# Kernel tuning notes

Hardware: AMD Instinct MI355X
Metric: run time of the kernel (lower is better)

## Reference

```python
import jax, jax.numpy as jnp
import numpy as np

N_IN = 8192
C_IN, C_H, C_OUT = 64, 32, 32
L = 3
GRID = 64  # parent grid extent (parents live on even coords of a 128^3 grid)


def _build_coords_and_maps():
    """Build sparse voxel coords and the 27-offset kernel map for 3x3x3 stride-1 convs."""
    rng = np.random.RandomState(0)
    pts = rng.randint(0, GRID, size=(4 * N_IN, 3))
    uniq = np.unique(pts, axis=0)
    parents = uniq[rng.permutation(uniq.shape[0])[:N_IN]] * 2  # stride-2 coords in [0,128)
    offs = np.array([[i, j, k] for i in (0, 1) for j in (0, 1) for k in (0, 1)])
    # generative conv transpose kernel=2 stride=2: child k of parent i sits at row i*8+k
    coords = (parents[:, None, :] + offs[None]).reshape(-1, 3)
    n_out = coords.shape[0]
    D = 2 * GRID
    grid = -np.ones((D, D, D), dtype=np.int64)
    grid[coords[:, 0], coords[:, 1], coords[:, 2]] = np.arange(n_out)
    k_offs = np.array([[i, j, k] for i in (-1, 0, 1) for j in (-1, 0, 1) for k in (-1, 0, 1)])
    ins, outs = [], []
    for d in k_offs:
        sh = coords + d
        valid = np.all((sh >= 0) & (sh < D), axis=1)
        j = -np.ones(n_out, dtype=np.int64)
        j[valid] = grid[sh[valid, 0], sh[valid, 1], sh[valid, 2]]
        m = j >= 0
        ins.append(j[m])
        outs.append(np.nonzero(m)[0])
    P = max(len(a) for a in ins)
    nbr_in = np.full((27, P), n_out, dtype=np.int32)   # pad -> dummy zero row
    nbr_out = np.full((27, P), n_out, dtype=np.int32)  # pad -> dummy dropped row
    for k in range(27):
        nbr_in[k, : len(ins[k])] = ins[k]
        nbr_out[k, : len(outs[k])] = outs[k]
    return jnp.asarray(nbr_in), jnp.asarray(nbr_out), n_out


def setup_inputs() -> dict:
    nbr_in, nbr_out, n_out = _build_coords_and_maps()
    key = jax.random.key(0)
    ks = jax.random.split(key, 20)
    w = lambda k, shape, fan: jax.random.normal(k, shape, jnp.float32) / np.float32(np.sqrt(fan))
    C4, C2 = C_OUT // 4, C_OUT // 2
    inp = {
        "x": jax.random.normal(ks[0], (N_IN, C_IN), jnp.float32),
        "W_up": w(ks[1], (8, C_IN, C_H), C_IN),
        "b_up": 0.01 * jax.random.normal(ks[2], (C_H,), jnp.float32),
        "W_conv": w(ks[3], (27, C_H, C_OUT), 27 * C_H),
        "b_conv": 0.01 * jax.random.normal(ks[4], (C_OUT,), jnp.float32),
        "Wb00": w(ks[5], (L, 27, C_OUT, C4), 27 * C_OUT),
        "bb00": 0.01 * jax.random.normal(ks[6], (L, C4), jnp.float32),
        "Wb01": w(ks[7], (L, 27, C4, C2), 27 * C4),
        "bb01": 0.01 * jax.random.normal(ks[8], (L, C2), jnp.float32),
        "Wb10": w(ks[9], (L, C_OUT, C4), C_OUT),
        "bb10": 0.01 * jax.random.normal(ks[10], (L, C4), jnp.float32),
        "Wb11": w(ks[11], (L, 27, C4, C4), 27 * C4),
        "bb11": 0.01 * jax.random.normal(ks[12], (L, C4), jnp.float32),
        "Wb12": w(ks[13], (L, C4, C2), C4),
        "bb12": 0.01 * jax.random.normal(ks[14], (L, C2), jnp.float32),
        "W_cls": w(ks[15], (27, C_OUT, 1), 27 * C_OUT),
        "b_cls": 0.01 * jax.random.normal(ks[16], (1,), jnp.float32),
        "nbr_in": nbr_in,
        "nbr_out": nbr_out,
        # ground-truth occupancy of out coords in target_label (precomputed set membership)
        "target": jax.random.bernoulli(ks[17], 0.5, (n_out,)),
    }
    return inp


def reference(x, W_up, b_up, W_conv, b_conv, Wb00, bb00, Wb01, bb01,
              Wb10, bb10, Wb11, bb11, Wb12, bb12, W_cls, b_cls,
              nbr_in, nbr_out, target):
    n_out = target.shape[0]
    r = jax.nn.relu

    def sconv(f, W, b):
        # 3x3x3 stride-1 sparse conv via shared kernel map: gather -> per-offset GEMM -> scatter-add
        fpad = jnp.concatenate([f, jnp.zeros((1, f.shape[1]), f.dtype)], axis=0)
        g = fpad[nbr_in]                                   # [27, P, Cin]
        contrib = jnp.einsum('kpc,kcd->kpd', g, W)         # [27, P, Cout]
        out = jnp.zeros((n_out + 1, W.shape[2]), f.dtype)
        out = out.at[nbr_out.reshape(-1)].add(contrib.reshape(-1, W.shape[2]))
        return out[:n_out] + b

    # generative transpose kernel=2 stride=2: child k of parent i -> row i*8+k
    up = (jnp.einsum('nc,kcd->nkd', x, W_up) + b_up).reshape(n_out, -1)
    out = r(sconv(r(up), W_conv, b_conv))
    for l in range(L):  # InceptionResNet blocks (PCGCv2-style)
        p0 = sconv(r(sconv(out, Wb00[l], bb00[l])), Wb01[l], bb01[l])
        p1 = r(out @ Wb10[l] + bb10[l])
        p1 = r(sconv(p1, Wb11[l], bb11[l]))
        p1 = p1 @ Wb12[l] + bb12[l]
        out = jnp.concatenate([p0, p1], axis=-1) + out
    out_cls = sconv(out, W_cls, b_cls)                     # [n_out, 1]
    score = out_cls[:, 0]
    keep = score > 0
    # topk(.,1) fallback when everything is negative
    fallback = keep | (jnp.arange(n_out) == jnp.argmax(score))
    keep = jnp.where(jnp.max(score) < 0, fallback, keep)
    # MinkowskiPruning with static shapes: zero-mask pruned rows
    out_pruned = out * keep[:, None].astype(out.dtype)
    return out_pruned, out_cls, target, keep
```

## Files before the change

### kernel.cpp

```cpp
#include <hip/hip_runtime.h>
#include <math.h>

static inline int cdiv(long long a, int b){ return (int)((a + b - 1) / b); }
#define DEVINL __device__ __forceinline__

DEVINL float4 relu4(const float* a){
  return make_float4(fmaxf(a[0],0.f), fmaxf(a[1],0.f), fmaxf(a[2],0.f), fmaxf(a[3],0.f));
}

DEVINL void load32(float* fv, const float* __restrict__ p){
#pragma unroll
  for (int q = 0; q < 8; ++q){
    float4 v = ((const float4*)p)[q];
    fv[4*q]=v.x; fv[4*q+1]=v.y; fv[4*q+2]=v.z; fv[4*q+3]=v.w;
  }
}
DEVINL void load8(float* fv, const float* __restrict__ p){
#pragma unroll
  for (int q = 0; q < 2; ++q){
    float4 v = ((const float4*)p)[q];
    fv[4*q]=v.x; fv[4*q+1]=v.y; fv[4*q+2]=v.z; fv[4*q+3]=v.w;
  }
}

DEVINL int sib_k(int o, int op){
  return 13 + 9*(((op>>2)&1) - ((o>>2)&1))
            + 3*(((op>>1)&1) - ((o>>1)&1))
            +   ((op&1) - (o&1));
}

__global__ void k_rinit(int* __restrict__ cnt, int n){
  int i = blockIdx.x*blockDim.x + threadIdx.x;
  if (i < n) cnt[i] = 0;
}

__global__ void k_rbuild(const int* __restrict__ nin, const int* __restrict__ nout,
                         int* __restrict__ cnt, int* __restrict__ rem, int P, int N){
  int p = blockIdx.x*blockDim.x + threadIdx.x;
  if (p >= 27*P) return;
  int oi = nout[p];
  if (oi >= N) return;
  int j = nin[p];
  if ((oi >> 3) == (j >> 3)) return;
  int k = p / P;
  int pos = atomicAdd(&cnt[oi], 1);
  rem[(size_t)oi*20 + pos] = (j << 5) | k;
}

__global__ __launch_bounds__(256) void k_up(const float* __restrict__ x,
    const float* __restrict__ Wup, const float* __restrict__ bup,
    float* __restrict__ f, int Nn){
  __shared__ float Ws[64*32];
  const int kk = blockIdx.y;
  for (int e = threadIdx.x*4; e < 2048; e += 1024)
    *(float4*)&Ws[e] = *(const float4*)&Wup[(size_t)kk*2048 + e];
  __syncthreads();
  int t = threadIdx.x, cg = t & 7, nr = t >> 3;
  int n = blockIdx.x*32 + nr, c0 = cg*4;
  float4 b4 = *(const float4*)(bup + c0);
  float acc[4] = {b4.x, b4.y, b4.z, b4.w};
  float xr[64];
  const float4* xp = (const float4*)(x + (size_t)n*64);
#pragma unroll
  for (int q = 0; q < 16; ++q){
    float4 v = xp[q];
    xr[4*q]=v.x; xr[4*q+1]=v.y; xr[4*q+2]=v.z; xr[4*q+3]=v.w;
  }
#pragma unroll
  for (int cc = 0; cc < 64; ++cc){
    float4 w = *(const float4*)(Ws + cc*32 + c0);
    acc[0]=fmaf(xr[cc],w.x,acc[0]); acc[1]=fmaf(xr[cc],w.y,acc[1]);
    acc[2]=fmaf(xr[cc],w.z,acc[2]); acc[3]=fmaf(xr[cc],w.w,acc[3]);
  }
  *(float4*)(f + ((size_t)n*8 + kk)*32 + c0) = relu4(acc);
}

__global__ __launch_bounds__(512) void k_conv1(const float* __restrict__ fin,
    const float* __restrict__ Wg, const float* __restrict__ bg,
    const int* __restrict__ cnt, const int* __restrict__ rem,
    float* __restrict__ fout, int N){
  __shared__ float Ws[27*516];
  const int ch = blockIdx.y;
  int t = threadIdx.x;
  for (int m = t; m < 3456; m += 512){
    int k = m >> 7, r = m & 127, cc = r >> 2, q = r & 3;
    *(float4*)&Ws[k*516 + cc*16 + q*4] =
      *(const float4*)&Wg[((size_t)(k*32 + cc))*32 + ch*16 + q*4];
  }
  __syncthreads();
  int cg = t & 3, r = t >> 2;
  int row = blockIdx.x*128 + r;
  int o = row & 7, base = row & ~7, c0 = cg*4;
  float4 b4 = *(const float4*)(bg + ch*16 + c0);
  float acc[4] = {b4.x,b4.y,b4.z,b4.w};
  float fv[32];
#pragma unroll
  for (int op = 0; op < 8; ++op){
    int kk = sib_k(o, op);
    load32(fv, fin + (size_t)(base+op)*32);
    const float* wk = Ws + kk*516 + c0;
#pragma unroll
    for (int cc = 0; cc < 32; ++cc){
      float4 w = *(const float4*)(wk + cc*16);
      acc[0]=fmaf(fv[cc],w.x,acc[0]); acc[1]=fmaf(fv[cc],w.y,acc[1]);
      acc[2]=fmaf(fv[cc],w.z,acc[2]); acc[3]=fmaf(fv[cc],w.w,acc[3]);
    }
  }
  int nrm = cnt[row];
  for (int s = 0; s < nrm; ++s){
    int e = rem[(size_t)row*20 + s];
    int kk = e & 31, j = e >> 5;
    load32(fv, fin + (size_t)j*32);
    const float* wk = Ws + kk*516 + c0;
#pragma unroll
    for (int cc = 0; cc < 32; ++cc){
      float4 w = *(const float4*)(wk + cc*16);
      acc[0]=fmaf(fv[cc],w.x,acc[0]); acc[1]=fmaf(fv[cc],w.y,acc[1]);
      acc[2]=fmaf(fv[cc],w.z,acc[2]); acc[3]=fmaf(fv[cc],w.w,acc[3]);
    }
  }
  *(float4*)(fout + (size_t)row*32 + ch*16 + c0) = relu4(acc);
}

__global__ __launch_bounds__(256) void k_blk_a(const float* __restrict__ fO,
    const float* __restrict__ W00, const float* __restrict__ b00,
    const float* __restrict__ W10, const float* __restrict__ b10,
    const int* __restrict__ cnt, const int* __restrict__ rem,
    float* __restrict__ a8, float* __restrict__ b8, int N){
  __shared__ float Ws[27*260 + 256];
  int t = threadIdx.x;
  for (int m = t; m < 1728; m += 256){
    int k = m >> 6, r = m & 63, cc = r >> 1, q = r & 1;
    *(float4*)&Ws[k*260 + cc*8 + q*4] = ((const float4*)W00)[m];
  }
  if (t < 64) *(float4*)&Ws[27*260 + t*4] = ((const float4*)W10)[t];
  __syncthreads();
  int cg = t & 1, r = t >> 1;
  int row = blockIdx.x*128 + r;
  int o = row & 7, base = row & ~7, c0 = cg*4;
  float4 b4 = *(const float4*)(b00 + c0);
  float acc[4] = {b4.x,b4.y,b4.z,b4.w};
  float fv[32];
#pragma unroll
  for (int op = 0; op < 8; ++op){
    int kk = sib_k(o, op);
    load32(fv, fO + (size_t)(base+op)*32);
    const float* wk = Ws + kk*260 + c0;
#pragma unroll
    for (int cc = 0; cc < 32; ++cc){
      float4 w = *(const float4*)(wk + cc*8);
      acc[0]=fmaf(fv[cc],w.x,acc[0]); acc[1]=fmaf(fv[cc],w.y,acc[1]);
      acc[2]=fmaf(fv[cc],w.z,acc[2]); acc[3]=fmaf(fv[cc],w.w,acc[3]);
    }
  }
  int nrm = cnt[row];
  for (int s = 0; s < nrm; ++s){
    int e = rem[(size_t)row*20 + s];
    int kk = e & 31, j = e >> 5;
    load32(fv, fO + (size_t)j*32);
    const float* wk = Ws + kk*260 + c0;
#pragma unroll
    for (int cc = 0; cc < 32; ++cc){
      float4 w = *(const float4*)(wk + cc*8);
      acc[0]=fmaf(fv[cc],w.x,acc[0]); acc[1]=fmaf(fv[cc],w.y,acc[1]);
      acc[2]=fmaf(fv[cc],w.z,acc[2]); acc[3]=fmaf(fv[cc],w.w,acc[3]);
    }
  }
  *(float4*)(a8 + (size_t)row*8 + c0) = relu4(acc);
  load32(fv, fO + (size_t)row*32);
  float4 d4 = *(const float4*)(b10 + c0);
  float accb[4] = {d4.x,d4.y,d4.z,d4.w};
#pragma unroll
  for (int cc = 0; cc < 32; ++cc){
    float4 w = *(const float4*)(Ws + 27*260 + cc*8 + c0);
    accb[0]=fmaf(fv[cc],w.x,accb[0]); accb[1]=fmaf(fv[cc],w.y,accb[1]);
    accb[2]=fmaf(fv[cc],w.z,accb[2]); accb[3]=fmaf(fv[cc],w.w,accb[3]);
  }
  *(float4*)(b8 + (size_t)row*8 + c0) = relu4(accb);
}

__global__ __launch_bounds__(256) void k_blk_b(const float* __restrict__ a8,
    const float* __restrict__ b8,
    const float* __restrict__ W01, const float* __restrict__ b01,
    const float* __restrict__ W11, const float* __restrict__ b11,
    const float* __restrict__ W12, const float* __restrict__ b12,
    const int* __restrict__ cnt, const int* __restrict__ rem,
    float* __restrict__ fout, int N){
  __shared__ float Ws[27*132 + 27*68 + 128];
  int t = threadIdx.x;
  for (int m = t; m < 864; m += 256){
    int k = m >> 5, r = m & 31, cc = r >> 2, q = r & 3;
    *(float4*)&Ws[k*132 + cc*16 + q*4] = ((const float4*)W01)[m];
  }
  for (int m = t; m < 432; m += 256){
    int k = m >> 4, r = m & 15, cc = r >> 1, q = r & 1;
    *(float4*)&Ws[3564 + k*68 + cc*8 + q*4] = ((const float4*)W11)[m];
  }
  if (t < 32) *(float4*)&Ws[5400 + t*4] = ((const float4*)W12)[t];
  __syncthreads();
  int cg = t & 3, r = t >> 2;
  int row = blockIdx.x*64 + r;
  int o = row & 7, base = row & ~7, c0 = cg*4;
  float4 b4 = *(const float4*)(b01 + c0);
  float acc0[4] = {b4.x,b4.y,b4.z,b4.w};
  float t8[8];
#pragma unroll
  for (int c = 0; c < 8; ++c) t8[c] = b11[c];
  float av[8], bv[8];
#pragma unroll
  for (int op = 0; op < 8; ++op){
    int kk = sib_k(o, op);
    load8(av, a8 + (size_t)(base+op)*8);
    load8(bv, b8 + (size_t)(base+op)*8);
    const float* w01k = Ws + kk*132 + c0;
    const float* w11k = Ws + 3564 + kk*68;
#pragma unroll
    for (int cc = 0; cc < 8; ++cc){
      float4 w = *(const float4*)(w01k + cc*16);
      acc0[0]=fmaf(av[cc],w.x,acc0[0]); acc0[1]=fmaf(av[cc],w.y,acc0[1]);
      acc0[2]=fmaf(av[cc],w.z,acc0[2]); acc0[3]=fmaf(av[cc],w.w,acc0[3]);
      float4 u0 = *(const float4*)(w11k + cc*8);
      float4 u1 = *(const float4*)(w11k + cc*8 + 4);
      t8[0]=fmaf(bv[cc],u0.x,t8[0]); t8[1]=fmaf(bv[cc],u0.y,t8[1]);
      t8[2]=fmaf(bv[cc],u0.z,t8[2]); t8[3]=fmaf(bv[cc],u0.w,t8[3]);
      t8[4]=fmaf(bv[cc],u1.x,t8[4]); t8[5]=fmaf(bv[cc],u1.y,t8[5]);
      t8[6]=fmaf(bv[cc],u1.z,t8[6]); t8[7]=fmaf(bv[cc],u1.w,t8[7]);
    }
  }
  int nrm = cnt[row];
  for (int s = 0; s < nrm; ++s){
    int e = rem[(size_t)row*20 + s];
    int kk = e & 31, j = e >> 5;
    load8(av, a8 + (size_t)j*8);
    load8(bv, b8 + (size_t)j*8);
    const float* w01k = Ws + kk*132 + c0;
    const float* w11k = Ws + 3564 + kk*68;
#pragma unroll
    for (int cc = 0; cc < 8; ++cc){
      float4 w = *(const float4*)(w01k + cc*16);
      acc0[0]=fmaf(av[cc],w.x,acc0[0]); acc0[1]=fmaf(av[cc],w.y,acc0[1]);
      acc0[2]=fmaf(av[cc],w.z,acc0[2]); acc0[3]=fmaf(av[cc],w.w,acc0[3]);
      float4 u0 = *(const float4*)(w11k + cc*8);
      float4 u1 = *(const float4*)(w11k + cc*8 + 4);
      t8[0]=fmaf(bv[cc],u0.x,t8[0]); t8[1]=fmaf(bv[cc],u0.y,t8[1]);
      t8[2]=fmaf(bv[cc],u0.z,t8[2]); t8[3]=fmaf(bv[cc],u0.w,t8[3]);
      t8[4]=fmaf(bv[cc],u1.x,t8[4]); t8[5]=fmaf(bv[cc],u1.y,t8[5]);
      t8[6]=fmaf(bv[cc],u1.z,t8[6]); t8[7]=fmaf(bv[cc],u1.w,t8[7]);
    }
  }
#pragma unroll
  for (int c = 0; c < 8; ++c) t8[c] = fmaxf(t8[c], 0.f);
  float4 d4 = *(const float4*)(b12 + c0);
  float acc1[4] = {d4.x,d4.y,d4.z,d4.w};
#pragma unroll
  for (int cc = 0; cc < 8; ++cc){
    float4 w = *(const float4*)(Ws + 5400 + cc*16 + c0);
    acc1[0]=fmaf(t8[cc],w.x,acc1[0]); acc1[1]=fmaf(t8[cc],w.y,acc1[1]);
    acc1[2]=fmaf(t8[cc],w.z,acc1[2]); acc1[3]=fmaf(t8[cc],w.w,acc1[3]);
  }
  float4* o0 = (float4*)(fout + (size_t)row*32 + c0);
  float4* o1 = (float4*)(fout + (size_t)row*32 + 16 + c0);
  float4 v0 = *o0, v1 = *o1;
  v0.x+=acc0[0]; v0.y+=acc0[1]; v0.z+=acc0[2]; v0.w+=acc0[3];
  v1.x+=acc1[0]; v1.y+=acc1[1]; v1.z+=acc1[2]; v1.w+=acc1[3];
  *o0 = v0; *o1 = v1;
}

__global__ __launch_bounds__(256) void k_cls(const float* __restrict__ fO,
    const float* __restrict__ Wc, const float* __restrict__ bc,
    const int* __restrict__ cnt, const int* __restrict__ rem,
    float* __restrict__ cls, int N){
  __shared__ float Ws[27*36];
  int t = threadIdx.x;
  if (t < 216){
    int k = t >> 3, r = t & 7;
    *(float4*)&Ws[k*36 + r*4] = ((const float4*)Wc)[t];
  }
  __syncthreads();
  int row = blockIdx.x*256 + t;
  int o = row & 7, base = row & ~7;
  float acc = 0.f;
  float fv[32];
#pragma unroll
  for (int op = 0; op < 8; ++op){
    int kk = sib_k(o, op);
    load32(fv, fO + (size_t)(base+op)*32);
    const float* wk = Ws + kk*36;
#pragma unroll
    for (int c4 = 0; c4 < 8; ++c4){
      float4 w = *(const float4*)(wk + c4*4);
      acc = fmaf(fv[4*c4],w.x,acc);   acc = fmaf(fv[4*c4+1],w.y,acc);
      acc = fmaf(fv[4*c4+2],w.z,acc); acc = fmaf(fv[4*c4+3],w.w,acc);
    }
  }
  int nrm = cnt[row];
  for (int s = 0; s < nrm; ++s){
    int e = rem[(size_t)row*20 + s];
    int kk = e & 31, j = e >> 5;
    load32(fv, fO + (size_t)j*32);
    const float* wk = Ws + kk*36;
#pragma unroll
    for (int c4 = 0; c4 < 8; ++c4){
      float4 w = *(const float4*)(wk + c4*4);
      acc = fmaf(fv[4*c4],w.x,acc);   acc = fmaf(fv[4*c4+1],w.y,acc);
      acc = fmaf(fv[4*c4+2],w.z,acc); acc = fmaf(fv[4*c4+3],w.w,acc);
    }
  }
  cls[row] = acc + bc[0];
}

__global__ void k_reduce1(const float* __restrict__ s, float* __restrict__ pmax,
                          int* __restrict__ pidx, int n){
  __shared__ float sm[256]; __shared__ int si[256];
  int t = threadIdx.x;
  float v = -INFINITY; int vi = 0x7fffffff;
  for (int j = blockIdx.x*256 + t; j < n; j += gridDim.x*256){
    float w = s[j];
    if (w > v){ v = w; vi = j; }
  }
  sm[t] = v; si[t] = vi; __syncthreads();
  for (int o = 128; o > 0; o >>= 1){
    if (t < o){
      if (sm[t+o] > sm[t] || (sm[t+o] == sm[t] && si[t+o] < si[t])){ sm[t]=sm[t+o]; si[t]=si[t+o]; }
    }
    __syncthreads();
  }
  if (t == 0){ pmax[blockIdx.x] = sm[0]; pidx[blockIdx.x] = si[0]; }
}

__global__ void k_reduce2(const float* __restrict__ pmax, const int* __restrict__ pidx,
                          float* __restrict__ g, int nb){
  __shared__ float sm[256]; __shared__ int si[256];
  int t = threadIdx.x;
  sm[t] = (t < nb) ? pmax[t] : -INFINITY;
  si[t] = (t < nb) ? pidx[t] : 0x7fffffff;
  __syncthreads();
  for (int o = 128; o > 0; o >>= 1){
    if (t < o){
      if (sm[t+o] > sm[t] || (sm[t+o] == sm[t] && si[t+o] < si[t])){ sm[t]=sm[t+o]; si[t]=si[t+o]; }
    }
    __syncthreads();
  }
  if (t == 0){ g[0] = sm[0]; ((int*)g)[1] = si[0]; }
}

__global__ void k_final(const float* __restrict__ out, const float* __restrict__ cls,
                        const int* __restrict__ target, const float* __restrict__ g,
                        float* __restrict__ dout, int n_out){
  int idx = blockIdx.x*blockDim.x + threadIdx.x;
  if (idx >= n_out*32) return;
  int row = idx >> 5, c = idx & 31;
  float s = cls[row];
  bool keep = s > 0.f;
  if (g[0] < 0.f) keep = keep || (row == ((const int*)g)[1]);
  float km = keep ? 1.f : 0.f;
  dout[idx] = out[idx] * km;
  if (c == 0){
    dout[(size_t)n_out*32 + row] = s;
    dout[(size_t)n_out*33 + row] = (target[row] != 0) ? 1.f : 0.f;
    dout[(size_t)n_out*34 + row] = km;
  }
}

extern "C" void kernel_launch(void* const* d_in, const int* in_sizes, int n_in,
                              void* d_out, int out_size, void* d_ws, size_t ws_size,
                              hipStream_t stream){
  const float* x      = (const float*)d_in[0];
  const float* W_up   = (const float*)d_in[1];
  const float* b_up   = (const float*)d_in[2];
  const float* W_conv = (const float*)d_in[3];
  const float* b_conv = (const float*)d_in[4];
  const float* Wb00   = (const float*)d_in[5];
  const float* bb00   = (const float*)d_in[6];
  const float* Wb01   = (const float*)d_in[7];
  const float* bb01   = (const float*)d_in[8];
  const float* Wb10   = (const float*)d_in[9];
  const float* bb10   = (const float*)d_in[10];
  const float* Wb11   = (const float*)d_in[11];
  const float* bb11   = (const float*)d_in[12];
  const float* Wb12   = (const float*)d_in[13];
  const float* bb12   = (const float*)d_in[14];
  const float* W_cls  = (const float*)d_in[15];
  const float* b_cls  = (const float*)d_in[16];
  const int*   nbr_in = (const int*)d_in[17];
  const int*   nbr_out= (const int*)d_in[18];
  const int*   target = (const int*)d_in[19];

  const int N = in_sizes[19];
  const int P = in_sizes[17] / 27;
  const int pairsT = 27 * P;
  const int Nn = N / 8;

  int*   cnt  = (int*)d_ws;
  int*   rem  = cnt + N;
  float* wsf  = (float*)(rem + (size_t)N*20);
  float* f_tmp = wsf;
  float* f_out = f_tmp + (size_t)N*32;
  float* a8    = f_out + (size_t)N*32;
  float* b8    = a8 + (size_t)N*8;
  float* cls   = b8 + (size_t)N*8;
  float* pmax  = cls + N;
  int*   pidx  = (int*)(pmax + 256);
  float* gm    = pmax + 512;

  const int B = 256;

  k_rinit<<<cdiv(N,B),B,0,stream>>>(cnt, N);
  k_rbuild<<<cdiv((long long)pairsT,B),B,0,stream>>>(nbr_in, nbr_out, cnt, rem, P, N);

  k_up<<<dim3(Nn/32,8),B,0,stream>>>(x, W_up, b_up, f_tmp, Nn);

  k_conv1<<<dim3(N/128,2),512,0,stream>>>(f_tmp, W_conv, b_conv, cnt, rem, f_out, N);

  for (int l = 0; l < 3; ++l){
    k_blk_a<<<N/128,B,0,stream>>>(f_out, Wb00 + (size_t)l*6912, bb00 + l*8,
                                  Wb10 + (size_t)l*256, bb10 + l*8, cnt, rem, a8, b8, N);
    k_blk_b<<<N/64,B,0,stream>>>(a8, b8,
                                 Wb01 + (size_t)l*3456, bb01 + l*16,
                                 Wb11 + (size_t)l*1728, bb11 + l*8,
                                 Wb12 + (size_t)l*128, bb12 + l*16,
                                 cnt, rem, f_out, N);
  }

  k_cls<<<N/256,B,0,stream>>>(f_out, W_cls, b_cls, cnt, rem, cls, N);

  k_reduce1<<<256,256,0,stream>>>(cls, pmax, pidx, N);
  k_reduce2<<<1,256,0,stream>>>(pmax, pidx, gm, 256);

  k_final<<<cdiv((long long)N*32,B),B,0,stream>>>(f_out, cls, target, gm, (float*)d_out, N);
}
```

Baseline: 213.9 us.

## Remap threads so each wavefront shares one child offset, drop smem padding

The sparse conv kernels now assign threads so that every wavefront of 64 lanes processes the same child index o across different parents. The sibling kernel offset kk is therefore uniform per wavefront, and weight reads from shared memory become broadcasts rather than divergent-address accesses. The shared weight arrays lose their padding to match. Block sizes grow to 512 threads and conv1 splits output channels four ways instead of two. The global feature loads become strided across parents (8 rows apart), which may reduce coalescing.

```diff
diff --git a/kernel.cpp b/kernel.cpp
--- a/kernel.cpp
+++ b/kernel.cpp
@@ -79,29 +79,29 @@
     const float* __restrict__ Wg, const float* __restrict__ bg,
     const int* __restrict__ cnt, const int* __restrict__ rem,
     float* __restrict__ fout, int N){
-  __shared__ float Ws[27*516];
-  const int ch = blockIdx.y;
-  int t = threadIdx.x;
-  for (int m = t; m < 3456; m += 512){
-    int k = m >> 7, r = m & 127, cc = r >> 2, q = r & 3;
-    *(float4*)&Ws[k*516 + cc*16 + q*4] =
-      *(const float4*)&Wg[((size_t)(k*32 + cc))*32 + ch*16 + q*4];
-  }
-  __syncthreads();
-  int cg = t & 3, r = t >> 2;
-  int row = blockIdx.x*128 + r;
-  int o = row & 7, base = row & ~7, c0 = cg*4;
-  float4 b4 = *(const float4*)(bg + ch*16 + c0);
+  __shared__ float Ws[27*32*8];
+  const int cb = blockIdx.y*8;
+  int t = threadIdx.x;
+  for (int m = t; m < 1728; m += 512){
+    int k = m >> 6, r = m & 63, cc = r >> 1, q = r & 1;
+    *(float4*)&Ws[k*256 + cc*8 + q*4] =
+      *(const float4*)&Wg[((size_t)(k*32 + cc))*32 + cb + q*4];
+  }
+  __syncthreads();
+  int o = t >> 6, lane = t & 63, p = lane >> 1, cg = lane & 1;
+  int base = blockIdx.x*256 + p*8;
+  int row = base + o, c0 = cg*4;
+  float4 b4 = *(const float4*)(bg + cb + c0);
   float acc[4] = {b4.x,b4.y,b4.z,b4.w};
   float fv[32];
 #pragma unroll
   for (int op = 0; op < 8; ++op){
     int kk = sib_k(o, op);
     load32(fv, fin + (size_t)(base+op)*32);
-    const float* wk = Ws + kk*516 + c0;
+    const float* wk = Ws + kk*256 + c0;
 #pragma unroll
     for (int cc = 0; cc < 32; ++cc){
-      float4 w = *(const float4*)(wk + cc*16);
+      float4 w = *(const float4*)(wk + cc*8);
       acc[0]=fmaf(fv[cc],w.x,acc[0]); acc[1]=fmaf(fv[cc],w.y,acc[1]);
       acc[2]=fmaf(fv[cc],w.z,acc[2]); acc[3]=fmaf(fv[cc],w.w,acc[3]);
     }
@@ -111,33 +111,33 @@
     int e = rem[(size_t)row*20 + s];
     int kk = e & 31, j = e >> 5;
     load32(fv, fin + (size_t)j*32);
-    const float* wk = Ws + kk*516 + c0;
+    const float* wk = Ws + kk*256 + c0;
 #pragma unroll
     for (int cc = 0; cc < 32; ++cc){
-      float4 w = *(const float4*)(wk + cc*16);
+      float4 w = *(const float4*)(wk + cc*8);
       acc[0]=fmaf(fv[cc],w.x,acc[0]); acc[1]=fmaf(fv[cc],w.y,acc[1]);
       acc[2]=fmaf(fv[cc],w.z,acc[2]); acc[3]=fmaf(fv[cc],w.w,acc[3]);
     }
   }
-  *(float4*)(fout + (size_t)row*32 + ch*16 + c0) = relu4(acc);
-}
-
-__global__ __launch_bounds__(256) void k_blk_a(const float* __restrict__ fO,
+  *(float4*)(fout + (size_t)row*32 + cb + c0) = relu4(acc);
+}
+
+__global__ __launch_bounds__(512) void k_blk_a(const float* __restrict__ fO,
     const float* __restrict__ W00, const float* __restrict__ b00,
     const float* __restrict__ W10, const float* __restrict__ b10,
     const int* __restrict__ cnt, const int* __restrict__ rem,
     float* __restrict__ a8, float* __restrict__ b8, int N){
-  __shared__ float Ws[27*260 + 256];
-  int t = threadIdx.x;
-  for (int m = t; m < 1728; m += 256){
+  __shared__ float Ws[27*256 + 256];
+  int t = threadIdx.x;
+  for (int m = t; m < 1728; m += 512){
     int k = m >> 6, r = m & 63, cc = r >> 1, q = r & 1;
-    *(float4*)&Ws[k*260 + cc*8 + q*4] = ((const float4*)W00)[m];
-  }
-  if (t < 64) *(float4*)&Ws[27*260 + t*4] = ((const float4*)W10)[t];
-  __syncthreads();
-  int cg = t & 1, r = t >> 1;
-  int row = blockIdx.x*128 + r;
-  int o = row & 7, base = row & ~7, c0 = cg*4;
+    *(float4*)&Ws[k*256 + cc*8 + q*4] = ((const float4*)W00)[m];
+  }
+  if (t < 64) *(float4*)&Ws[6912 + t*4] = ((const float4*)W10)[t];
+  __syncthreads();
+  int o = t >> 6, lane = t & 63, p = lane >> 1, cg = lane & 1;
+  int base = blockIdx.x*256 + p*8;
+  int row = base + o, c0 = cg*4;
   float4 b4 = *(const float4*)(b00 + c0);
   float acc[4] = {b4.x,b4.y,b4.z,b4.w};
   float fv[32];
@@ -145,7 +145,7 @@
   for (int op = 0; op < 8; ++op){
     int kk = sib_k(o, op);
     load32(fv, fO + (size_t)(base+op)*32);
-    const float* wk = Ws + kk*260 + c0;
+    const float* wk = Ws + kk*256 + c0;
 #pragma unroll
     for (int cc = 0; cc < 32; ++cc){
       float4 w = *(const float4*)(wk + cc*8);
@@ -158,7 +158,7 @@
     int e = rem[(size_t)row*20 + s];
     int kk = e & 31, j = e >> 5;
     load32(fv, fO + (size_t)j*32);
-    const float* wk = Ws + kk*260 + c0;
+    const float* wk = Ws + kk*256 + c0;
 #pragma unroll
     for (int cc = 0; cc < 32; ++cc){
       float4 w = *(const float4*)(wk + cc*8);
@@ -172,35 +172,31 @@
   float accb[4] = {d4.x,d4.y,d4.z,d4.w};
 #pragma unroll
   for (int cc = 0; cc < 32; ++cc){
-    float4 w = *(const float4*)(Ws + 27*260 + cc*8 + c0);
+    float4 w = *(const float4*)(Ws + 6912 + cc*8 + c0);
     accb[0]=fmaf(fv[cc],w.x,accb[0]); accb[1]=fmaf(fv[cc],w.y,accb[1]);
     accb[2]=fmaf(fv[cc],w.z,accb[2]); accb[3]=fmaf(fv[cc],w.w,accb[3]);
   }
   *(float4*)(b8 + (size_t)row*8 + c0) = relu4(accb);
 }
 
-__global__ __launch_bounds__(256) void k_blk_b(const float* __restrict__ a8,
+__global__ __launch_bounds__(512) void k_blk_b(const float* __restrict__ a8,
     const float* __restrict__ b8,
     const float* __restrict__ W01, const float* __restrict__ b01,
     const float* __restrict__ W11, const float* __restrict__ b11,
     const float* __restrict__ W12, const float* __restrict__ b12,
     const int* __restrict__ cnt, const int* __restrict__ rem,
     float* __restrict__ fout, int N){
-  __shared__ float Ws[27*132 + 27*68 + 128];
-  int t = threadIdx.x;
-  for (int m = t; m < 864; m += 256){
-    int k = m >> 5, r = m & 31, cc = r >> 2, q = r & 3;
-    *(float4*)&Ws[k*132 + cc*16 + q*4] = ((const float4*)W01)[m];
-  }
-  for (int m = t; m < 432; m += 256){
-    int k = m >> 4, r = m & 15, cc = r >> 1, q = r & 1;
-    *(float4*)&Ws[3564 + k*68 + cc*8 + q*4] = ((const float4*)W11)[m];
-  }
-  if (t < 32) *(float4*)&Ws[5400 + t*4] = ((const float4*)W12)[t];
-  __syncthreads();
-  int cg = t & 3, r = t >> 2;
-  int row = blockIdx.x*64 + r;
-  int o = row & 7, base = row & ~7, c0 = cg*4;
+  __shared__ float Ws[27*128 + 27*64 + 128];
+  int t = threadIdx.x;
+  for (int m = t; m < 864; m += 512)
+    ((float4*)Ws)[m] = ((const float4*)W01)[m];
+  for (int m = t; m < 432; m += 512)
+    ((float4*)(Ws + 3456))[m] = ((const float4*)W11)[m];
+  if (t < 32) *(float4*)&Ws[5184 + t*4] = ((const float4*)W12)[t];
+  __syncthreads();
+  int o = t >> 6, lane = t & 63, p = lane >> 2, cg = lane & 3;
+  int base = blockIdx.x*128 + p*8;
+  int row = base + o, c0 = cg*4;
   float4 b4 = *(const float4*)(b01 + c0);
   float acc0[4] = {b4.x,b4.y,b4.z,b4.w};
   float t8[8];
@@ -212,8 +208,8 @@
     int kk = sib_k(o, op);
     load8(av, a8 + (size_t)(base+op)*8);
     load8(bv, b8 + (size_t)(base+op)*8);
-    const float* w01k = Ws + kk*132 + c0;
-    const float* w11k = Ws + 3564 + kk*68;
+    const float* w01k = Ws + kk*128 + c0;
+    const float* w11k = Ws + 3456 + kk*64;
 #pragma unroll
     for (int cc = 0; cc < 8; ++cc){
       float4 w = *(const float4*)(w01k + cc*16);
@@ -233,8 +229,8 @@
     int kk = e & 31, j = e >> 5;
     load8(av, a8 + (size_t)j*8);
     load8(bv, b8 + (size_t)j*8);
-    const float* w01k = Ws + kk*132 + c0;
-    const float* w11k = Ws + 3564 + kk*68;
+    const float* w01k = Ws + kk*128 + c0;
+    const float* w11k = Ws + 3456 + kk*64;
 #pragma unroll
     for (int cc = 0; cc < 8; ++cc){
       float4 w = *(const float4*)(w01k + cc*16);
@@ -254,7 +250,7 @@
   float acc1[4] = {d4.x,d4.y,d4.z,d4.w};
 #pragma unroll
   for (int cc = 0; cc < 8; ++cc){
-    float4 w = *(const float4*)(Ws + 5400 + cc*16 + c0);
+    float4 w = *(const float4*)(Ws + 5184 + cc*16 + c0);
     acc1[0]=fmaf(t8[cc],w.x,acc1[0]); acc1[1]=fmaf(t8[cc],w.y,acc1[1]);
     acc1[2]=fmaf(t8[cc],w.z,acc1[2]); acc1[3]=fmaf(t8[cc],w.w,acc1[3]);
   }
@@ -270,22 +266,20 @@
     const float* __restrict__ Wc, const float* __restrict__ bc,
     const int* __restrict__ cnt, const int* __restrict__ rem,
     float* __restrict__ cls, int N){
-  __shared__ float Ws[27*36];
-  int t = threadIdx.x;
-  if (t < 216){
-    int k = t >> 3, r = t & 7;
-    *(float4*)&Ws[k*36 + r*4] = ((const float4*)Wc)[t];
-  }
-  __syncthreads();
-  int row = blockIdx.x*256 + t;
-  int o = row & 7, base = row & ~7;
+  __shared__ float Ws[27*32];
+  int t = threadIdx.x;
+  if (t < 216) ((float4*)Ws)[t] = ((const float4*)Wc)[t];
+  __syncthreads();
+  int o = blockIdx.y*4 + (t >> 6), p = t & 63;
+  int base = (blockIdx.x*64 + p)*8;
+  int row = base + o;
   float acc = 0.f;
   float fv[32];
 #pragma unroll
   for (int op = 0; op < 8; ++op){
     int kk = sib_k(o, op);
     load32(fv, fO + (size_t)(base+op)*32);
-    const float* wk = Ws + kk*36;
+    const float* wk = Ws + kk*32;
 #pragma unroll
     for (int c4 = 0; c4 < 8; ++c4){
       float4 w = *(const float4*)(wk + c4*4);
@@ -298,7 +292,7 @@
     int e = rem[(size_t)row*20 + s];
     int kk = e & 31, j = e >> 5;
     load32(fv, fO + (size_t)j*32);
-    const float* wk = Ws + kk*36;
+    const float* wk = Ws + kk*32;
 #pragma unroll
     for (int c4 = 0; c4 < 8; ++c4){
       float4 w = *(const float4*)(wk + c4*4);
@@ -410,19 +404,19 @@
 
   k_up<<<dim3(Nn/32,8),B,0,stream>>>(x, W_up, b_up, f_tmp, Nn);
 
-  k_conv1<<<dim3(N/128,2),512,0,stream>>>(f_tmp, W_conv, b_conv, cnt, rem, f_out, N);
+  k_conv1<<<dim3(N/256,4),512,0,stream>>>(f_tmp, W_conv, b_conv, cnt, rem, f_out, N);
 
   for (int l = 0; l < 3; ++l){
-    k_blk_a<<<N/128,B,0,stream>>>(f_out, Wb00 + (size_t)l*6912, bb00 + l*8,
-                                  Wb10 + (size_t)l*256, bb10 + l*8, cnt, rem, a8, b8, N);
-    k_blk_b<<<N/64,B,0,stream>>>(a8, b8,
-                                 Wb01 + (size_t)l*3456, bb01 + l*16,
-                                 Wb11 + (size_t)l*1728, bb11 + l*8,
-                                 Wb12 + (size_t)l*128, bb12 + l*16,
-                                 cnt, rem, f_out, N);
-  }
-
-  k_cls<<<N/256,B,0,stream>>>(f_out, W_cls, b_cls, cnt, rem, cls, N);
+    k_blk_a<<<N/256,512,0,stream>>>(f_out, Wb00 + (size_t)l*6912, bb00 + l*8,
+                                    Wb10 + (size_t)l*256, bb10 + l*8, cnt, rem, a8, b8, N);
+    k_blk_b<<<N/128,512,0,stream>>>(a8, b8,
+                                    Wb01 + (size_t)l*3456, bb01 + l*16,
+                                    Wb11 + (size_t)l*1728, bb11 + l*8,
+                                    Wb12 + (size_t)l*128, bb12 + l*16,
+                                    cnt, rem, f_out, N);
+  }
+
+  k_cls<<<dim3(N/512,2),B,0,stream>>>(f_out, W_cls, b_cls, cnt, rem, cls, N);
 
   k_reduce1<<<256,256,0,stream>>>(cls, pmax, pidx, N);
   k_reduce2<<<1,256,0,stream>>>(pmax, pidx, gm, 256);
```

After: 217.7 us. Within noise of the previous version (+1.8%).
